# Kernel tuning notes

Hardware: AMD Instinct MI355X
Metric: run time of the kernel (lower is better)

Reference implementation:

```python
import jax, jax.numpy as jnp
import numpy as np

ITERATIONS = 5
B, N, M = 32, 2048, 2048


def vec2mat(trans):
    # trans: [B, 3] = [theta, tx, ty] -> [B, 3, 3] homogeneous transform
    c = jnp.cos(trans[:, 0])
    s = jnp.sin(trans[:, 0])
    tx, ty = trans[:, 1], trans[:, 2]
    z = jnp.zeros_like(c)
    o = jnp.ones_like(c)
    row0 = jnp.stack([c, -s, tx], axis=-1)
    row1 = jnp.stack([s, c, ty], axis=-1)
    row2 = jnp.stack([z, z, o], axis=-1)
    return jnp.stack([row0, row1, row2], axis=1)


def setup_inputs() -> dict:
    key = jax.random.key(0)
    k1, k2, k3 = jax.random.split(key, 3)
    source = jax.random.normal(k1, (B, N, 2), dtype=jnp.float32)
    target = jax.random.normal(k2, (B, M, 2), dtype=jnp.float32)
    init_transformation = jax.random.normal(k3, (B, 3), dtype=jnp.float32)
    return {"source": source, "target": target,
            "init_transformation": init_transformation}


def reference(source, target, init_transformation):
    T = vec2mat(init_transformation)  # [B,3,3]

    def apply_T(T):
        # equivalent to [source | 1] @ T^T, keeping xy columns
        R = T[:, :2, :2]
        t = T[:, :2, 2]
        return jnp.einsum('bnd,bed->bne', source, R) + t[:, None, :]

    st = apply_T(T)  # transformed source, [B,N,2]
    t_sq = jnp.sum(target ** 2, axis=-1)  # [B,M]

    for _ in range(ITERATIONS):
        # squared euclidean distances via ||s||^2 + ||t||^2 - 2 s.t (avoids [B,N,M,2])
        s_sq = jnp.sum(st ** 2, axis=-1)  # [B,N]
        cross = jnp.einsum('bnd,bmd->bnm', st, target)
        dists = s_sq[:, :, None] + t_sq[:, None, :] - 2.0 * cross  # [B,N,M]
        weights = jax.nn.softmax(-dists, axis=-1)
        target_corr = jnp.einsum('bnm,bmd->bnd', weights, target)  # [B,N,2]

        centroid_s = jnp.mean(st, axis=1, keepdims=True)          # [B,1,2]
        centroid_t = jnp.mean(target_corr, axis=1, keepdims=True)  # [B,1,2]
        H = jnp.einsum('bnd,bne->bde', st - centroid_s, target_corr - centroid_t)  # [B,2,2]

        U, S, Vh = jnp.linalg.svd(H, full_matrices=False)
        V = jnp.swapaxes(Vh, -1, -2)
        R_delta = V @ jnp.swapaxes(U, -1, -2)  # [B,2,2]
        t_delta = jnp.swapaxes(centroid_t, 1, 2) - R_delta @ jnp.swapaxes(centroid_s, 1, 2)  # [B,2,1]

        delta_theta = jnp.arctan2(R_delta[:, 1, 0], R_delta[:, 0, 0])
        delta_vec = jnp.stack([delta_theta, t_delta[:, 0, 0], t_delta[:, 1, 0]], axis=1)
        T = vec2mat(delta_vec) @ T
        st = apply_T(T)

    refined = jnp.stack([jnp.arctan2(T[:, 1, 0], T[:, 0, 0]),
                         T[:, 0, 2], T[:, 1, 2]], axis=1)
    return refined
```

## Files before the change

kernel.cpp:

```cpp
#include <hip/hip_runtime.h>
#include <math.h>

#define BN 32
#define NPTS 2048
#define MPTS 2048
#define ITERS 5
#define LOG2E 1.44269504088896340736f
#define SHIFT_C 14.0f

typedef _Float16 v8h __attribute__((ext_vector_type(8)));
typedef _Float16 v4h __attribute__((ext_vector_type(4)));
typedef __fp16   f16x2 __attribute__((ext_vector_type(2)));
typedef float    v4f __attribute__((ext_vector_type(4)));

#define T_OFF    0
#define PART_OFF 256
#define P1_OFF   8192
#define P2_OFF   (8192 + BN * 2048 * 4)

__global__ __launch_bounds__(512, 4) void icp_pass(const float* __restrict__ source,
                                                   float* __restrict__ ws) {
    __shared__ v8h A1s[2050];
    __shared__ v8h A2s[516];
    __shared__ float4 comb[8][4][16];
    __shared__ float red[2][8];
    const int tid = threadIdx.x;
    const int wv  = tid >> 6;
    const int l   = tid & 63;
    const int q   = l >> 4;
    const int col = l & 15;
    const int wq  = wv & 3;
    const int rg  = wv >> 2;
    const int b   = blockIdx.x & 31;
    const int gg  = blockIdx.x >> 5;
    const int g   = gg * 2 + rg;

    const _Float16 h0 = (_Float16)0.0f;
    const _Float16 h1 = (_Float16)1.0f;

    const float4* g1 = (const float4*)(ws + P1_OFF) + (size_t)b * 2048;
    float4* s1 = (float4*)A1s;
#pragma unroll
    for (int i = 0; i < 4; ++i) s1[tid + i * 512] = g1[tid + i * 512];
    const float4* g2 = (const float4*)(ws + P2_OFF) + (size_t)b * 512;
    ((float4*)A2s)[tid] = g2[tid];
    if (tid == 0) {
        A1s[2048] = (v8h){h1, h1, h0, h0, h0, h0, h0, h0};
        A1s[2049] = (v8h){h0, h0, h0, h0, h0, h0, h0, h0};
        A2s[512]  = (v8h){h1, h1, h1, h1, h0, h0, h0, h0};
        A2s[513]  = (v8h){h0, h0, h0, h0, h0, h0, h0, h0};
    }

    const float* T = ws + T_OFF + b * 6;
    const float r00 = T[0], r01 = T[1], tx = T[2];
    const float r10 = T[3], r11 = T[4], ty = T[5];

    v8h B1[4];
#pragma unroll
    for (int nt = 0; nt < 4; ++nt) {
        const int row = g * 64 + nt * 16 + col;
        const float2 sp = ((const float2*)source)[b * NPTS + row];
        const float sx = fmaf(r00, sp.x, fmaf(r01, sp.y, tx));
        const float sy = fmaf(r10, sp.x, fmaf(r11, sp.y, ty));
        const float qpx = 2.0f * LOG2E * sx;
        const float qpy = 2.0f * LOG2E * sy;
        const float rc  = SHIFT_C - LOG2E * fmaf(sx, sx, sy * sy);
        const _Float16 qpxh = (_Float16)qpx;
        const _Float16 qpxl = (_Float16)(qpx - (float)qpxh);
        const _Float16 qpyh = (_Float16)qpy;
        const _Float16 qpyl = (_Float16)(qpy - (float)qpyh);
        const _Float16 rch  = (_Float16)rc;
        const _Float16 rcl  = (_Float16)(rc - (float)rch);
        v8h f;
        if (q == 0)      f = (v8h){qpxh, qpxl, qpxh, qpyh, qpyl, qpyh, h1, h1};
        else if (q == 1) f = (v8h){rch, rcl, h0, h0, h0, h0, h0, h0};
        else             f = (v8h){h0, h0, h0, h0, h0, h0, h0, h0};
        B1[nt] = f;
    }
    __syncthreads();

    const char* A1c = (const char*)A1s;
    const char* A2c = (const char*)A2s;
    int ad1 = (q == 0) ? (wq * 512 + col) * 16 : ((q == 1) ? 2048 * 16 : 2049 * 16);
    const int st1 = (q == 0) ? 256 : 0;
    int ad2 = (col == 1) ? (wq * 2048 + q * 16)
            : (col == 2) ? (wq * 2048 + q * 16 + 8)
            : ((col == 0) ? 512 * 16 : 513 * 16);
    const int st2 = (col == 1 || col == 2) ? 64 : 0;
    const v4f zero4 = (v4f){0.f, 0.f, 0.f, 0.f};

    v4f D2[4];
#pragma unroll
    for (int nt = 0; nt < 4; ++nt) D2[nt] = zero4;

    v8h a1w[32];
    v4h a2w[32];
    v4f D1w[32][4];
    a1w[0] = *(const v8h*)(A1c + ad1); a2w[0] = *(const v4h*)(A2c + ad2);
    ad1 += st1; ad2 += st2;
    a1w[1] = *(const v8h*)(A1c + ad1); a2w[1] = *(const v4h*)(A2c + ad2);
    ad1 += st1; ad2 += st2;
#pragma unroll
    for (int nt = 0; nt < 4; ++nt)
        D1w[0][nt] = __builtin_amdgcn_mfma_f32_16x16x32_f16(a1w[0], B1[nt], zero4, 0, 0, 0);

#pragma unroll
    for (int t = 0; t < 32; ++t) {
        if (t < 30) {
            a1w[t + 2] = *(const v8h*)(A1c + ad1);
            a2w[t + 2] = *(const v4h*)(A2c + ad2);
            ad1 += st1; ad2 += st2;
        }
        if (t < 31) {
#pragma unroll
            for (int nt = 0; nt < 4; ++nt)
                D1w[t + 1][nt] = __builtin_amdgcn_mfma_f32_16x16x32_f16(a1w[t + 1], B1[nt], zero4, 0, 0, 0);
        }
        float e[16];
#pragma unroll
        for (int nt = 0; nt < 4; ++nt)
#pragma unroll
            for (int j = 0; j < 4; ++j)
                e[nt * 4 + j] = __builtin_amdgcn_exp2f(D1w[t][nt][j]);
#pragma unroll
        for (int nt = 0; nt < 4; ++nt) {
            union { v4h v; f16x2 h[2]; } u;
            u.h[0] = __builtin_amdgcn_cvt_pkrtz(e[nt * 4 + 0], e[nt * 4 + 1]);
            u.h[1] = __builtin_amdgcn_cvt_pkrtz(e[nt * 4 + 2], e[nt * 4 + 3]);
            D2[nt] = __builtin_amdgcn_mfma_f32_16x16x16f16(a2w[t], u.v, D2[nt], 0, 0, 0);
        }
    }

    if (l < 16) {
#pragma unroll
        for (int nt = 0; nt < 4; ++nt)
            comb[wv][nt][col] = make_float4(D2[nt][0], D2[nt][1], D2[nt][2], 0.f);
    }
    __syncthreads();
    float den = 0.f, ax = 0.f, ay = 0.f;
#pragma unroll
    for (int w = 0; w < 4; ++w) {
        const float4 p = comb[rg * 4 + w][q][col];
        den += p.x; ax += p.y; ay += p.z;
    }
    const float tcx = ax / den;
    const float tcy = ay / den;
    const int erow = g * 64 + q * 16 + col;
    const float2 sp = ((const float2*)source)[b * NPTS + erow];
    const float sx = fmaf(r00, sp.x, fmaf(r01, sp.y, tx));
    const float sy = fmaf(r10, sp.x, fmaf(r11, sp.y, ty));
    float v[8] = {sx, sy, tcx, tcy, sx * tcx, sx * tcy, sy * tcx, sy * tcy};
#pragma unroll
    for (int off = 32; off > 0; off >>= 1) {
#pragma unroll
        for (int j = 0; j < 8; ++j) v[j] += __shfl_xor(v[j], off, 64);
    }
    if (l == 0 && wq == 0) {
#pragma unroll
        for (int j = 0; j < 8; ++j) red[rg][j] = v[j];
    }
    __syncthreads();
    if (tid < 8) {
        float* slot = ws + PART_OFF + ((size_t)b * 16 + gg) * 8;
        slot[tid] = red[0][tid] + red[1][tid];
    }
}

__global__ __launch_bounds__(256) void icp_T(float* __restrict__ ws,
                                             float* __restrict__ out,
                                             int last) {
    __shared__ float a[BN][8];
    const int t = threadIdx.x;
    {
        const int bb = t >> 3, j = t & 7;
        const float* base = ws + PART_OFF + (size_t)bb * 128 + j;
        float s = 0.f;
#pragma unroll
        for (int s16 = 0; s16 < 16; ++s16) s += base[s16 * 8];
        a[bb][j] = s;
    }
    __syncthreads();
    if (t < BN) {
        const int b = t;
        const float Ssx = a[b][0], Ssy = a[b][1], Stcx = a[b][2], Stcy = a[b][3];
        const float Sxx = a[b][4], Sxy = a[b][5], Syx = a[b][6], Syy = a[b][7];
        const float invN = 1.0f / (float)NPTS;
        const float csx = Ssx * invN, csy = Ssy * invN;
        const float ctx = Stcx * invN, cty = Stcy * invN;
        const float Hxx = Sxx - Ssx * ctx;
        const float Hxy = Sxy - Ssx * cty;
        const float Hyx = Syx - Ssy * ctx;
        const float Hyy = Syy - Ssy * cty;
        const float aa = Hxx, bb2 = Hyx, cc = Hxy, dd = Hyy;
        const float det = aa * dd - bb2 * cc;
        const bool refl = (det < 0.f);
        const float xr = refl ? (aa - dd) : (aa + dd);
        const float yr = refl ? (bb2 + cc) : (cc - bb2);
        const float r = fmaxf(sqrtf(xr * xr + yr * yr), 1e-30f);
        const float R00 = xr / r, R10 = yr / r;
        const float R01 = refl ? R10 : -R10;
        const float R11 = refl ? -R00 : R00;
        const float tdx = ctx - (R00 * csx + R01 * csy);
        const float tdy = cty - (R10 * csx + R11 * csy);
        const float cD = R00, sD = R10;
        float* Tw = ws + T_OFF + b * 6;
        const float o00 = Tw[0], o01 = Tw[1], otx = Tw[2];
        const float o10 = Tw[3], o11 = Tw[4], oty = Tw[5];
        const float n00 = cD * o00 - sD * o10;
        const float n01 = cD * o01 - sD * o11;
        const float ntx = cD * otx - sD * oty + tdx;
        const float n10 = sD * o00 + cD * o10;
        const float n11 = sD * o01 + cD * o11;
        const float nty = sD * otx + cD * oty + tdy;
        Tw[0] = n00; Tw[1] = n01; Tw[2] = ntx;
        Tw[3] = n10; Tw[4] = n11; Tw[5] = nty;
        if (last) {
            out[b * 3 + 0] = atan2f(n10, n00);
            out[b * 3 + 1] = ntx;
            out[b * 3 + 2] = nty;
        }
    }
}

__global__ __launch_bounds__(256) void icp_init(const float* __restrict__ target,
                                                const float* __restrict__ init_t,
                                                float* __restrict__ ws) {
    const int b = blockIdx.x;
    const int tid = threadIdx.x;
    if (tid == 0) {
        const float th = init_t[b * 3 + 0];
        const float c = cosf(th), s = sinf(th);
        float* Tw = ws + T_OFF + b * 6;
        Tw[0] = c;  Tw[1] = -s; Tw[2] = init_t[b * 3 + 1];
        Tw[3] = s;  Tw[4] = c;  Tw[5] = init_t[b * 3 + 2];
    }
    const float2* tg = (const float2*)target + b * MPTS;
    v8h* P1 = (v8h*)(ws + P1_OFF) + (size_t)b * MPTS;
#pragma unroll
    for (int i = 0; i < 8; ++i) {
        const int m = tid + i * 256;
        const float2 k = tg[m];
        const float bm = -LOG2E * fmaf(k.x, k.x, k.y * k.y);
        const _Float16 kxh = (_Float16)k.x;
        const _Float16 kxl = (_Float16)(k.x - (float)kxh);
        const _Float16 kyh = (_Float16)k.y;
        const _Float16 kyl = (_Float16)(k.y - (float)kyh);
        const _Float16 bmh = (_Float16)bm;
        const _Float16 bml = (_Float16)(bm - (float)bmh);
        P1[m] = (v8h){kxh, kxh, kxl, kyh, kyh, kyl, bmh, bml};
    }
    v8h* P2 = (v8h*)(ws + P2_OFF) + (size_t)b * 512;
#pragma unroll
    for (int i = 0; i < 2; ++i) {
        const int e = tid + i * 256;
        const int m0 = e * 4;
        const float2 k0 = tg[m0 + 0];
        const float2 k1 = tg[m0 + 1];
        const float2 k2 = tg[m0 + 2];
        const float2 k3 = tg[m0 + 3];
        P2[e] = (v8h){(_Float16)k0.x, (_Float16)k1.x, (_Float16)k2.x, (_Float16)k3.x,
                      (_Float16)k0.y, (_Float16)k1.y, (_Float16)k2.y, (_Float16)k3.y};
    }
}

extern "C" void kernel_launch(void* const* d_in, const int* in_sizes, int n_in,
                              void* d_out, int out_size, void* d_ws, size_t ws_size,
                              hipStream_t stream) {
    const float* source = (const float*)d_in[0];
    const float* target = (const float*)d_in[1];
    const float* initt  = (const float*)d_in[2];
    float* out = (float*)d_out;
    float* ws  = (float*)d_ws;

    icp_init<<<BN, 256, 0, stream>>>(target, initt, ws);
    for (int k = 0; k < ITERS; ++k) {
        icp_pass<<<BN * 16, 512, 0, stream>>>(source, ws);
        icp_T<<<1, 256, 0, stream>>>(ws, out, k == ITERS - 1);
    }
}
```

Before: 162.5 us.

## Fuse target packing and Kabsch update into pass kernel, drop init/T launches

Removes the separate init kernel and the per-iteration single-block transform kernel. Each pass block now packs the fp16 target operands straight into LDS from the raw target, and reduces the previous iteration's partials to compute the new transform itself. Per-iteration partials and transforms go to separate workspace slots so blocks never race. This cuts the launch count from 11 to 6 and drops the workspace round-trip for packed targets, at the cost of redundant packing and Kabsch math in every block.

Result: faster. 157.1 us (-3.3%).

```diff
diff --git a/kernel.cpp b/kernel.cpp
--- a/kernel.cpp
+++ b/kernel.cpp
@@ -13,17 +13,51 @@
 typedef __fp16   f16x2 __attribute__((ext_vector_type(2)));
 typedef float    v4f __attribute__((ext_vector_type(4)));
 
-#define T_OFF    0
-#define PART_OFF 256
-#define P1_OFF   8192
-#define P2_OFF   (8192 + BN * 2048 * 4)
+#define TS_OFF   0
+#define PART_OFF 2048
+
+__device__ __forceinline__ void kabsch_compose(const float* a8,
+                                               float& Tc, float& Ts,
+                                               float& Ttx, float& Tty) {
+    const float Ssx = a8[0], Ssy = a8[1], Stcx = a8[2], Stcy = a8[3];
+    const float Sxx = a8[4], Sxy = a8[5], Syx = a8[6], Syy = a8[7];
+    const float invN = 1.0f / (float)NPTS;
+    const float csx = Ssx * invN, csy = Ssy * invN;
+    const float ctx = Stcx * invN, cty = Stcy * invN;
+    const float Hxx = Sxx - Ssx * ctx;
+    const float Hxy = Sxy - Ssx * cty;
+    const float Hyx = Syx - Ssy * ctx;
+    const float Hyy = Syy - Ssy * cty;
+    const float a = Hxx, bb = Hyx, cc = Hxy, d = Hyy;
+    const float det = a * d - bb * cc;
+    const bool refl = (det < 0.f);
+    const float xr = refl ? (a - d) : (a + d);
+    const float yr = refl ? (bb + cc) : (cc - bb);
+    const float r = fmaxf(sqrtf(xr * xr + yr * yr), 1e-30f);
+    const float R00 = xr / r, R10 = yr / r;
+    const float R01 = refl ? R10 : -R10;
+    const float R11 = refl ? -R00 : R00;
+    const float tdx = ctx - (R00 * csx + R01 * csy);
+    const float tdy = cty - (R10 * csx + R11 * csy);
+    const float cD = R00, sD = R10;
+    const float nC  = cD * Tc - sD * Ts;
+    const float nS  = sD * Tc + cD * Ts;
+    const float nTx = cD * Ttx - sD * Tty + tdx;
+    const float nTy = sD * Ttx + cD * Tty + tdy;
+    Tc = nC; Ts = nS; Ttx = nTx; Tty = nTy;
+}
 
 __global__ __launch_bounds__(512, 4) void icp_pass(const float* __restrict__ source,
-                                                   float* __restrict__ ws) {
+                                                   const float* __restrict__ target,
+                                                   const float* __restrict__ init_t,
+                                                   float* __restrict__ ws,
+                                                   int iter) {
     __shared__ v8h A1s[2050];
     __shared__ v8h A2s[516];
     __shared__ float4 comb[8][4][16];
     __shared__ float red[2][8];
+    __shared__ float shT[6];
+    __shared__ float pacc[128];
     const int tid = threadIdx.x;
     const int wv  = tid >> 6;
     const int l   = tid & 63;
@@ -38,12 +72,29 @@
     const _Float16 h0 = (_Float16)0.0f;
     const _Float16 h1 = (_Float16)1.0f;
 
-    const float4* g1 = (const float4*)(ws + P1_OFF) + (size_t)b * 2048;
-    float4* s1 = (float4*)A1s;
-#pragma unroll
-    for (int i = 0; i < 4; ++i) s1[tid + i * 512] = g1[tid + i * 512];
-    const float4* g2 = (const float4*)(ws + P2_OFF) + (size_t)b * 512;
-    ((float4*)A2s)[tid] = g2[tid];
+    const float2* tg = (const float2*)target + b * MPTS;
+#pragma unroll
+    for (int i = 0; i < 4; ++i) {
+        const int m = tid + i * 512;
+        const float2 k = tg[m];
+        const float bm = -LOG2E * fmaf(k.x, k.x, k.y * k.y);
+        const _Float16 kxh = (_Float16)k.x;
+        const _Float16 kxl = (_Float16)(k.x - (float)kxh);
+        const _Float16 kyh = (_Float16)k.y;
+        const _Float16 kyl = (_Float16)(k.y - (float)kyh);
+        const _Float16 bmh = (_Float16)bm;
+        const _Float16 bml = (_Float16)(bm - (float)bmh);
+        A1s[m] = (v8h){kxh, kxh, kxl, kyh, kyh, kyl, bmh, bml};
+    }
+    if (tid < 512) {
+        const int e = tid;
+        const float2 k0 = tg[e * 4 + 0];
+        const float2 k1 = tg[e * 4 + 1];
+        const float2 k2 = tg[e * 4 + 2];
+        const float2 k3 = tg[e * 4 + 3];
+        A2s[e] = (v8h){(_Float16)k0.x, (_Float16)k1.x, (_Float16)k2.x, (_Float16)k3.x,
+                       (_Float16)k0.y, (_Float16)k1.y, (_Float16)k2.y, (_Float16)k3.y};
+    }
     if (tid == 0) {
         A1s[2048] = (v8h){h1, h1, h0, h0, h0, h0, h0, h0};
         A1s[2049] = (v8h){h0, h0, h0, h0, h0, h0, h0, h0};
@@ -51,9 +102,42 @@
         A2s[513]  = (v8h){h0, h0, h0, h0, h0, h0, h0, h0};
     }
 
-    const float* T = ws + T_OFF + b * 6;
-    const float r00 = T[0], r01 = T[1], tx = T[2];
-    const float r10 = T[3], r11 = T[4], ty = T[5];
+    if (iter == 0) {
+        if (tid == 0) {
+            const float th = init_t[b * 3 + 0];
+            const float c = cosf(th), s = sinf(th);
+            shT[0] = c; shT[1] = -s; shT[2] = init_t[b * 3 + 1];
+            shT[3] = s; shT[4] = c;  shT[5] = init_t[b * 3 + 2];
+            float* Tw = ws + TS_OFF + b * 6;
+            Tw[0] = shT[0]; Tw[1] = shT[1]; Tw[2] = shT[2];
+            Tw[3] = shT[3]; Tw[4] = shT[4]; Tw[5] = shT[5];
+        }
+    } else {
+        if (tid < 128)
+            pacc[tid] = ws[PART_OFF + (size_t)(iter - 1) * BN * 128 + b * 128 + tid];
+        __syncthreads();
+        if (tid == 0) {
+            float a8[8];
+#pragma unroll
+            for (int j = 0; j < 8; ++j) {
+                float s = 0.f;
+#pragma unroll
+                for (int s16 = 0; s16 < 16; ++s16) s += pacc[s16 * 8 + j];
+                a8[j] = s;
+            }
+            const float* Tp = ws + TS_OFF + (iter - 1) * 192 + b * 6;
+            float Tc = Tp[0], Ts = Tp[3], Ttx = Tp[2], Tty = Tp[5];
+            kabsch_compose(a8, Tc, Ts, Ttx, Tty);
+            shT[0] = Tc; shT[1] = -Ts; shT[2] = Ttx;
+            shT[3] = Ts; shT[4] = Tc;  shT[5] = Tty;
+            float* Tw = ws + TS_OFF + iter * 192 + b * 6;
+            Tw[0] = Tc; Tw[1] = -Ts; Tw[2] = Ttx;
+            Tw[3] = Ts; Tw[4] = Tc;  Tw[5] = Tty;
+        }
+    }
+    __syncthreads();
+    const float r00 = shT[0], r01 = shT[1], tx = shT[2];
+    const float r10 = shT[3], r11 = shT[4], ty = shT[5];
 
     v8h B1[4];
 #pragma unroll
@@ -160,107 +244,30 @@
         for (int j = 0; j < 8; ++j) red[rg][j] = v[j];
     }
     __syncthreads();
-    if (tid < 8) {
-        float* slot = ws + PART_OFF + ((size_t)b * 16 + gg) * 8;
-        slot[tid] = red[0][tid] + red[1][tid];
-    }
-}
-
-__global__ __launch_bounds__(256) void icp_T(float* __restrict__ ws,
-                                             float* __restrict__ out,
-                                             int last) {
-    __shared__ float a[BN][8];
-    const int t = threadIdx.x;
-    {
-        const int bb = t >> 3, j = t & 7;
-        const float* base = ws + PART_OFF + (size_t)bb * 128 + j;
-        float s = 0.f;
-#pragma unroll
-        for (int s16 = 0; s16 < 16; ++s16) s += base[s16 * 8];
-        a[bb][j] = s;
-    }
-    __syncthreads();
-    if (t < BN) {
-        const int b = t;
-        const float Ssx = a[b][0], Ssy = a[b][1], Stcx = a[b][2], Stcy = a[b][3];
-        const float Sxx = a[b][4], Sxy = a[b][5], Syx = a[b][6], Syy = a[b][7];
-        const float invN = 1.0f / (float)NPTS;
-        const float csx = Ssx * invN, csy = Ssy * invN;
-        const float ctx = Stcx * invN, cty = Stcy * invN;
-        const float Hxx = Sxx - Ssx * ctx;
-        const float Hxy = Sxy - Ssx * cty;
-        const float Hyx = Syx - Ssy * ctx;
-        const float Hyy = Syy - Ssy * cty;
-        const float aa = Hxx, bb2 = Hyx, cc = Hxy, dd = Hyy;
-        const float det = aa * dd - bb2 * cc;
-        const bool refl = (det < 0.f);
-        const float xr = refl ? (aa - dd) : (aa + dd);
-        const float yr = refl ? (bb2 + cc) : (cc - bb2);
-        const float r = fmaxf(sqrtf(xr * xr + yr * yr), 1e-30f);
-        const float R00 = xr / r, R10 = yr / r;
-        const float R01 = refl ? R10 : -R10;
-        const float R11 = refl ? -R00 : R00;
-        const float tdx = ctx - (R00 * csx + R01 * csy);
-        const float tdy = cty - (R10 * csx + R11 * csy);
-        const float cD = R00, sD = R10;
-        float* Tw = ws + T_OFF + b * 6;
-        const float o00 = Tw[0], o01 = Tw[1], otx = Tw[2];
-        const float o10 = Tw[3], o11 = Tw[4], oty = Tw[5];
-        const float n00 = cD * o00 - sD * o10;
-        const float n01 = cD * o01 - sD * o11;
-        const float ntx = cD * otx - sD * oty + tdx;
-        const float n10 = sD * o00 + cD * o10;
-        const float n11 = sD * o01 + cD * o11;
-        const float nty = sD * otx + cD * oty + tdy;
-        Tw[0] = n00; Tw[1] = n01; Tw[2] = ntx;
-        Tw[3] = n10; Tw[4] = n11; Tw[5] = nty;
-        if (last) {
-            out[b * 3 + 0] = atan2f(n10, n00);
-            out[b * 3 + 1] = ntx;
-            out[b * 3 + 2] = nty;
-        }
-    }
-}
-
-__global__ __launch_bounds__(256) void icp_init(const float* __restrict__ target,
-                                                const float* __restrict__ init_t,
-                                                float* __restrict__ ws) {
-    const int b = blockIdx.x;
-    const int tid = threadIdx.x;
-    if (tid == 0) {
-        const float th = init_t[b * 3 + 0];
-        const float c = cosf(th), s = sinf(th);
-        float* Tw = ws + T_OFF + b * 6;
-        Tw[0] = c;  Tw[1] = -s; Tw[2] = init_t[b * 3 + 1];
-        Tw[3] = s;  Tw[4] = c;  Tw[5] = init_t[b * 3 + 2];
-    }
-    const float2* tg = (const float2*)target + b * MPTS;
-    v8h* P1 = (v8h*)(ws + P1_OFF) + (size_t)b * MPTS;
-#pragma unroll
-    for (int i = 0; i < 8; ++i) {
-        const int m = tid + i * 256;
-        const float2 k = tg[m];
-        const float bm = -LOG2E * fmaf(k.x, k.x, k.y * k.y);
-        const _Float16 kxh = (_Float16)k.x;
-        const _Float16 kxl = (_Float16)(k.x - (float)kxh);
-        const _Float16 kyh = (_Float16)k.y;
-        const _Float16 kyl = (_Float16)(k.y - (float)kyh);
-        const _Float16 bmh = (_Float16)bm;
-        const _Float16 bml = (_Float16)(bm - (float)bmh);
-        P1[m] = (v8h){kxh, kxh, kxl, kyh, kyh, kyl, bmh, bml};
-    }
-    v8h* P2 = (v8h*)(ws + P2_OFF) + (size_t)b * 512;
-#pragma unroll
-    for (int i = 0; i < 2; ++i) {
-        const int e = tid + i * 256;
-        const int m0 = e * 4;
-        const float2 k0 = tg[m0 + 0];
-        const float2 k1 = tg[m0 + 1];
-        const float2 k2 = tg[m0 + 2];
-        const float2 k3 = tg[m0 + 3];
-        P2[e] = (v8h){(_Float16)k0.x, (_Float16)k1.x, (_Float16)k2.x, (_Float16)k3.x,
-                      (_Float16)k0.y, (_Float16)k1.y, (_Float16)k2.y, (_Float16)k3.y};
-    }
+    if (tid < 2) {
+        float4* slot = (float4*)(ws + PART_OFF + (size_t)iter * BN * 128 + b * 128 + gg * 8);
+        slot[tid] = make_float4(red[0][tid * 4 + 0] + red[1][tid * 4 + 0],
+                                red[0][tid * 4 + 1] + red[1][tid * 4 + 1],
+                                red[0][tid * 4 + 2] + red[1][tid * 4 + 2],
+                                red[0][tid * 4 + 3] + red[1][tid * 4 + 3]);
+    }
+}
+
+__global__ __launch_bounds__(64) void icp_finish(float* __restrict__ out,
+                                                 const float* __restrict__ ws) {
+    const int b = threadIdx.x;
+    if (b >= BN) return;
+    const float* base = ws + PART_OFF + (size_t)(ITERS - 1) * BN * 128 + b * 128;
+    float a8[8] = {0.f, 0.f, 0.f, 0.f, 0.f, 0.f, 0.f, 0.f};
+    for (int s16 = 0; s16 < 16; ++s16)
+#pragma unroll
+        for (int j = 0; j < 8; ++j) a8[j] += base[s16 * 8 + j];
+    const float* Tp = ws + TS_OFF + (ITERS - 1) * 192 + b * 6;
+    float Tc = Tp[0], Ts = Tp[3], Ttx = Tp[2], Tty = Tp[5];
+    kabsch_compose(a8, Tc, Ts, Ttx, Tty);
+    out[b * 3 + 0] = atan2f(Ts, Tc);
+    out[b * 3 + 1] = Ttx;
+    out[b * 3 + 2] = Tty;
 }
 
 extern "C" void kernel_launch(void* const* d_in, const int* in_sizes, int n_in,
@@ -272,9 +279,7 @@
     float* out = (float*)d_out;
     float* ws  = (float*)d_ws;
 
-    icp_init<<<BN, 256, 0, stream>>>(target, initt, ws);
-    for (int k = 0; k < ITERS; ++k) {
-        icp_pass<<<BN * 16, 512, 0, stream>>>(source, ws);
-        icp_T<<<1, 256, 0, stream>>>(ws, out, k == ITERS - 1);
-    }
-}
+    for (int k = 0; k < ITERS; ++k)
+        icp_pass<<<BN * 16, 512, 0, stream>>>(source, target, initt, ws, k);
+    icp_finish<<<1, 64, 0, stream>>>(out, ws);
+}
```
